# Kernel tuning notes

Hardware: AMD Instinct MI355X
Metric: run time of the kernel (lower is better)

The kernel has to match this reference:

```python
import jax, jax.numpy as jnp
import numpy as np

D_MODEL = 128
NEG_INF = -1e30


def setup_inputs() -> dict:
    key = jax.random.key(0)
    k1, k2, k3, k4 = jax.random.split(key, 4)
    B, Lc, Lq, d = 32, 2048, 256, D_MODEL
    C = jax.random.normal(k1, (B, Lc, d), dtype=jnp.float32)
    Q = jax.random.normal(k2, (B, Lq, d), dtype=jnp.float32)
    # Linear(3d, 1): weight laid out for cat order (Q_, C_, C_*Q_)
    w = jax.random.normal(k3, (3 * d,), dtype=jnp.float32) / np.sqrt(3 * d)
    b = jax.random.normal(k4, (1,), dtype=jnp.float32) * 0.01
    c_mask = jnp.ones((B, Lc), dtype=jnp.int32)
    q_mask = jnp.ones((B, Lq), dtype=jnp.int32)
    return {"C": C, "Q": Q, "w": w, "b": b, "c_mask": c_mask, "q_mask": q_mask}


def reference(C, Q, w, b, c_mask, q_mask):
    d = C.shape[-1]
    # Algebraic decomposition of Linear([Q_, C_, C_*Q_]) -> scalar:
    # S[b,i,j] = Q[b,j]@w_q + C[b,i]@w_c + (C[b,i]*w_m)@Q[b,j] + bias
    w_q, w_c, w_m = w[:d], w[d:2 * d], w[2 * d:]
    S = (C @ w_c)[:, :, None] \
        + (Q @ w_q)[:, None, :] \
        + jnp.einsum('bid,bjd->bij', C * w_m, Q) \
        + b[0]                                        # (B, Lc, Lq)
    mask = (c_mask[:, :, None] * q_mask[:, None, :]).astype(S.dtype)
    S = S * mask + NEG_INF * (1.0 - mask)
    S1 = jax.nn.softmax(S, axis=1)  # softmax over context dim (as in source)
    S2 = jax.nn.softmax(S, axis=2)  # softmax over query dim
    C2Q = jnp.einsum('bij,bjd->bid', S1, Q)           # (B, Lc, d)
    # Q2C = S1 @ S2^T @ C, associated as S1 @ (S2^T @ C) to avoid (Lc,Lc)
    T = jnp.einsum('bkj,bkd->bjd', S2, C)             # (B, Lq, d)
    Q2C = jnp.einsum('bij,bjd->bid', S1, T)           # (B, Lc, d)
    out = jnp.concatenate([C, C2Q, C * C2Q, C * Q2C], axis=2)  # (B, Lc, 4d)
    # dropout omitted (deterministic reference / eval mode)
    return out
```

## Files before the change

### kernel.cpp

```cpp
#include <hip/hip_runtime.h>


#define LC 2048
#define LQ 256
#define DM 128
#define NEG_INF_F (-1e30f)

using bf16x8  = __attribute__((ext_vector_type(8))) __bf16;
using f32x4   = __attribute__((ext_vector_type(4))) float;
using ushort8 = __attribute__((ext_vector_type(8))) unsigned short;

__device__ __forceinline__ unsigned short f2bf(float x) {
    unsigned int u = __float_as_uint(x);
    u += 0x7fffu + ((u >> 16) & 1u);
    return (unsigned short)(u >> 16);
}
__device__ __forceinline__ float bf2f(unsigned short h) {
    return __uint_as_float(((unsigned int)h) << 16);
}
__device__ __forceinline__ f32x4 mfma16(bf16x8 a, bf16x8 b, f32x4 c) {
    return __builtin_amdgcn_mfma_f32_16x16x32_bf16(a, b, c, 0, 0, 0);
}

__global__ __launch_bounds__(256) void k_preQ(const float* __restrict__ Q,
        const float* __restrict__ w, unsigned short* __restrict__ Qbf,
        unsigned short* __restrict__ Qt, float* __restrict__ rq) {
    const int b = blockIdx.z, j0 = blockIdx.x * 64, d0 = blockIdx.y * 64;
    const int tid = threadIdx.x;
    __shared__ float tile[64][65];
    __shared__ float wq[128];
    if (tid < 128) wq[tid] = w[tid];
    __syncthreads();
    const int r = tid >> 2, c0 = (tid & 3) * 16;
    const float4* sp = (const float4*)(Q + (size_t)(b * LQ + j0 + r) * DM + d0 + c0);
    float v[16];
#pragma unroll
    for (int u = 0; u < 4; ++u) {
        float4 t = sp[u];
        v[4*u] = t.x; v[4*u+1] = t.y; v[4*u+2] = t.z; v[4*u+3] = t.w;
    }
    unsigned short ob[16];
    float p = 0.f;
#pragma unroll
    for (int u = 0; u < 16; ++u) {
        ob[u] = f2bf(v[u]);
        p += v[u] * wq[d0 + c0 + u];
        tile[r][c0 + u] = v[u];
    }
    ushort8* qb = (ushort8*)(Qbf + (size_t)(b * LQ + j0 + r) * DM + d0 + c0);
    qb[0] = *(ushort8*)&ob[0];
    qb[1] = *(ushort8*)&ob[8];
    p += __shfl_xor(p, 1);
    p += __shfl_xor(p, 2);
    if ((tid & 3) == 0) atomicAdd(&rq[b * LQ + j0 + r], p);
    __syncthreads();
    unsigned short o[16];
#pragma unroll
    for (int u = 0; u < 16; ++u) o[u] = f2bf(tile[c0 + u][r]);
    ushort8* dp = (ushort8*)(Qt + (size_t)(b * DM + d0 + r) * LQ + j0 + c0);
    dp[0] = *(ushort8*)&o[0];
    dp[1] = *(ushort8*)&o[8];
}

__global__ __launch_bounds__(256) void k_preC(const float* __restrict__ C,
        unsigned short* __restrict__ Ct) {
    const int b = blockIdx.z, i0 = blockIdx.x * 64, d0 = blockIdx.y * 64;
    const int tid = threadIdx.x;
    __shared__ float tile[64][65];
    const int r = tid >> 2, c0 = (tid & 3) * 16;
    const float4* sp = (const float4*)(C + (size_t)(b * LC + i0 + r) * DM + d0 + c0);
#pragma unroll
    for (int u = 0; u < 4; ++u) {
        float4 t = sp[u];
        tile[r][c0 + 4*u] = t.x; tile[r][c0 + 4*u + 1] = t.y;
        tile[r][c0 + 4*u + 2] = t.z; tile[r][c0 + 4*u + 3] = t.w;
    }
    __syncthreads();
    unsigned short o[16];
#pragma unroll
    for (int u = 0; u < 16; ++u) o[u] = f2bf(tile[c0 + u][r]);
    ushort8* dp = (ushort8*)(Ct + (size_t)(b * DM + d0 + r) * LC + i0 + c0);
    dp[0] = *(ushort8*)&o[0];
    dp[1] = *(ushort8*)&o[8];
}

__global__ __launch_bounds__(256) void k1_scores(
    const float* __restrict__ C, const unsigned short* __restrict__ Qbf,
    const float* __restrict__ w, const float* __restrict__ bptr,
    const int* __restrict__ c_mask, const int* __restrict__ q_mask,
    const float* __restrict__ rq,
    unsigned short* __restrict__ E, float* __restrict__ l1g, float* __restrict__ l2g) {
    const int b = blockIdx.y;
    const int i0 = blockIdx.x * 64;
    const int tid = threadIdx.x;
    const int lane = tid & 63, wid = tid >> 6;
    const int quad = lane >> 4, l15 = lane & 15;

    __shared__ unsigned short Alds[64][136];
    __shared__ float wsm[256];
    __shared__ float rcs[64], rqs[256], cms[64], qms[256], l2s[64];
    __shared__ float b0s;

    if (tid < 256) {
        wsm[tid] = w[128 + tid];
        rqs[tid] = rq[b * LQ + tid];
        qms[tid] = (float)q_mask[b * LQ + tid];
    }
    if (tid < 64) {
        cms[tid] = (float)c_mask[b * LC + i0 + tid];
        l2s[tid] = 0.f;
    }
    if (tid == 0) b0s = bptr[0];
    __syncthreads();

    {
        const int r = tid >> 2, qq = tid & 3;
        const float4* cp = (const float4*)(C + (size_t)(b * LC + i0 + r) * DM + qq * 32);
        float prc = 0.f;
#pragma unroll
        for (int u = 0; u < 8; ++u) {
            float4 v = cp[u];
            const int c0 = qq * 32 + u * 4;
            prc += v.x * wsm[c0] + v.y * wsm[c0 + 1] + v.z * wsm[c0 + 2] + v.w * wsm[c0 + 3];
            Alds[r][c0 + 0] = f2bf(v.x * wsm[128 + c0]);
            Alds[r][c0 + 1] = f2bf(v.y * wsm[129 + c0]);
            Alds[r][c0 + 2] = f2bf(v.z * wsm[130 + c0]);
            Alds[r][c0 + 3] = f2bf(v.w * wsm[131 + c0]);
        }
        prc += __shfl_xor(prc, 1);
        prc += __shfl_xor(prc, 2);
        if (qq == 0) rcs[r] = prc;
    }
    __syncthreads();

    const int n_base = wid * 64;
    const unsigned short* qbase = Qbf + (size_t)b * LQ * DM;
    const f32x4 z4 = {0.f, 0.f, 0.f, 0.f};
    f32x4 acc[4][4];
#pragma unroll
    for (int mt = 0; mt < 4; ++mt)
#pragma unroll
        for (int nt = 0; nt < 4; ++nt) acc[mt][nt] = z4;

#pragma unroll
    for (int kc = 0; kc < 4; ++kc) {
        const int ko = kc * 32 + quad * 8;
        bf16x8 af[4], bfr[4];
#pragma unroll
        for (int mt = 0; mt < 4; ++mt)
            af[mt] = *(const bf16x8*)&Alds[mt * 16 + l15][ko];
#pragma unroll
        for (int nt = 0; nt < 4; ++nt)
            bfr[nt] = *(const bf16x8*)(qbase + (size_t)(n_base + nt * 16 + l15) * DM + ko);
#pragma unroll
        for (int mt = 0; mt < 4; ++mt)
#pragma unroll
            for (int nt = 0; nt < 4; ++nt)
                acc[mt][nt] = mfma16(af[mt], bfr[nt], acc[mt][nt]);
    }

    const float b0 = b0s;
    float colsum[4] = {0.f, 0.f, 0.f, 0.f};
#pragma unroll
    for (int mt = 0; mt < 4; ++mt) {
#pragma unroll
        for (int reg = 0; reg < 4; ++reg) {
            const int m = mt * 16 + quad * 4 + reg;
            float rowsum = 0.f;
#pragma unroll
            for (int nt = 0; nt < 4; ++nt) {
                const int n = n_base + nt * 16 + l15;
                float s = acc[mt][nt][reg] + rcs[m] + rqs[n] + b0;
                const float mk = cms[m] * qms[n];
                s = s * mk + NEG_INF_F * (1.f - mk);
                const float e = __expf(s);
                acc[mt][nt][reg] = e;
                rowsum += e;
                colsum[nt] += e;
            }
            rowsum += __shfl_xor(rowsum, 1);
            rowsum += __shfl_xor(rowsum, 2);
            rowsum += __shfl_xor(rowsum, 4);
            rowsum += __shfl_xor(rowsum, 8);
            if (l15 == 0) atomicAdd(&l2s[m], rowsum);
        }
    }
#pragma unroll
    for (int nt = 0; nt < 4; ++nt) {
        float v = colsum[nt];
        v += __shfl_xor(v, 16);
        v += __shfl_xor(v, 32);
        if (quad == 0) atomicAdd(&l1g[b * LQ + n_base + nt * 16 + l15], v);
    }
    __syncthreads();
    if (tid < 64) l2g[b * LC + i0 + tid] = l2s[tid];

#pragma unroll
    for (int mt = 0; mt < 4; ++mt) {
#pragma unroll
        for (int reg = 0; reg < 4; ++reg) {
            const int m = mt * 16 + quad * 4 + reg;
            const float rl = 1.0f / l2s[m];
            unsigned short* erow = E + (size_t)(b * LC + i0 + m) * LQ;
#pragma unroll
            for (int nt = 0; nt < 4; ++nt) {
                const int n = n_base + nt * 16 + l15;
                erow[n] = f2bf(acc[mt][nt][reg] * rl);
            }
        }
    }
}

__global__ __launch_bounds__(256) void kS_scaleQt(
    const unsigned short* __restrict__ Qt, const float* __restrict__ l1g,
    unsigned short* __restrict__ Qts) {
    const int b = blockIdx.y;
    const int tid = threadIdx.x;
    __shared__ float rl1s[256];
    rl1s[tid] = 1.0f / l1g[b * LQ + tid];
    __syncthreads();
    const int idx = blockIdx.x * 256 + tid;
    const int d = idx >> 5, jc = (idx & 31) * 8;
    const ushort8 v = *(const ushort8*)(Qt + (size_t)(b * DM + d) * LQ + jc);
    unsigned short o[8];
#pragma unroll
    for (int u = 0; u < 8; ++u) o[u] = f2bf(bf2f(v[u]) * rl1s[jc + u]);
    *(ushort8*)(Qts + (size_t)(b * DM + d) * LQ + jc) = *(ushort8*)&o[0];
}

__global__ __launch_bounds__(512) void k3_Tt(
    const unsigned short* __restrict__ E, const unsigned short* __restrict__ Ct,
    const float* __restrict__ l1g, unsigned short* __restrict__ Tt) {
    const int j0 = blockIdx.x * 64, d0 = blockIdx.y * 64, b = blockIdx.z;
    const int tid = threadIdx.x;
    const int lane = tid & 63, wid = tid >> 6;
    const int quad = lane >> 4, l15 = lane & 15;
    const int m_base = (wid >> 1) * 16, n32 = (wid & 1) * 32;

    __shared__ unsigned short Ab[64][136];
    __shared__ unsigned short Bb[64][136];
    __shared__ float rl1s[64];
    if (tid < 64) rl1s[tid] = 1.0f / l1g[b * LQ + j0 + tid];

    const f32x4 z4 = {0.f, 0.f, 0.f, 0.f};
    f32x4 acc[2] = {z4, z4};

    for (int it = 0; it < 16; ++it) {
        const int ic = it * 128;
        __syncthreads();
        {
            const int r = tid >> 3, q = tid & 7;
            const ushort8* cp = (const ushort8*)(Ct + (size_t)(b * DM + d0 + r) * LC + ic + q * 16);
            *(ushort8*)&Ab[r][q * 16] = cp[0];
            *(ushort8*)&Ab[r][q * 16 + 8] = cp[1];
        }
        {
            const int il = tid >> 2, sg = (tid & 3) * 16;
            const ushort8* ep = (const ushort8*)(E + (size_t)(b * LC + ic + il) * LQ + j0 + sg);
            ushort8 e0 = ep[0], e1 = ep[1];
#pragma unroll
            for (int u = 0; u < 8; ++u) Bb[sg + u][il] = e0[u];
#pragma unroll
            for (int u = 0; u < 8; ++u) Bb[sg + 8 + u][il] = e1[u];
        }
        __syncthreads();
#pragma unroll
        for (int kk = 0; kk < 4; ++kk) {
            const int ko = kk * 32 + quad * 8;
            bf16x8 af = *(const bf16x8*)&Ab[m_base + l15][ko];
            bf16x8 b0f = *(const bf16x8*)&Bb[n32 + l15][ko];
            bf16x8 b1f = *(const bf16x8*)&Bb[n32 + 16 + l15][ko];
            acc[0] = mfma16(af, b0f, acc[0]);
            acc[1] = mfma16(af, b1f, acc[1]);
        }
    }
#pragma unroll
    for (int nt = 0; nt < 2; ++nt)
#pragma unroll
        for (int reg = 0; reg < 4; ++reg) {
            const int dd = d0 + m_base + quad * 4 + reg;
            const int jl = n32 + nt * 16 + l15;
            Tt[(size_t)(b * DM + dd) * LQ + j0 + jl] = f2bf(acc[nt][reg] * rl1s[jl]);
        }
}

__global__ __launch_bounds__(256) void k4_out(
    const unsigned short* __restrict__ E, const float* __restrict__ C,
    const unsigned short* __restrict__ Qts, const unsigned short* __restrict__ Tt,
    const float* __restrict__ l2g, float* __restrict__ out) {
    const int b = blockIdx.y;
    const int i0 = blockIdx.x * 64;
    const int tid = threadIdx.x;
    const int lane = tid & 63, wid = tid >> 6;
    const int quad = lane >> 4, l15 = lane & 15;
    const int n_base = wid * 32;

    __shared__ unsigned short Aq[64][72];
    __shared__ unsigned short Bq[128][72];
    __shared__ unsigned short Bt2[128][72];
    __shared__ float l2s[64];
    if (tid < 64) l2s[tid] = l2g[b * LC + i0 + tid];

    const f32x4 z4 = {0.f, 0.f, 0.f, 0.f};
    f32x4 acc1[4][2], acc2[4][2];
#pragma unroll
    for (int mt = 0; mt < 4; ++mt)
#pragma unroll
        for (int nt = 0; nt < 2; ++nt) { acc1[mt][nt] = z4; acc2[mt][nt] = z4; }

#pragma unroll 1
    for (int kc = 0; kc < 4; ++kc) {
        const int jc = kc * 64;
        __syncthreads();
        {
            const int r = tid >> 2, q = tid & 3;
            const ushort8* ep = (const ushort8*)(E + (size_t)(b * LC + i0 + r) * LQ + jc + q * 16);
            *(ushort8*)&Aq[r][q * 16] = ep[0];
            *(ushort8*)&Aq[r][q * 16 + 8] = ep[1];
        }
        {
            const int r = tid >> 1, h = (tid & 1) * 32;
            const ushort8* qp = (const ushort8*)(Qts + (size_t)(b * DM + r) * LQ + jc + h);
            const ushort8* tp = (const ushort8*)(Tt + (size_t)(b * DM + r) * LQ + jc + h);
#pragma unroll
            for (int u = 0; u < 4; ++u) {
                *(ushort8*)&Bq[r][h + u * 8] = qp[u];
                *(ushort8*)&Bt2[r][h + u * 8] = tp[u];
            }
        }
        __syncthreads();
#pragma unroll
        for (int kk = 0; kk < 2; ++kk) {
            const int ko = kk * 32 + quad * 8;
            bf16x8 a[4], bq[2], bt[2];
#pragma unroll
            for (int mt = 0; mt < 4; ++mt)
                a[mt] = *(const bf16x8*)&Aq[mt * 16 + l15][ko];
#pragma unroll
            for (int nt = 0; nt < 2; ++nt) {
                bq[nt] = *(const bf16x8*)&Bq[n_base + nt * 16 + l15][ko];
                bt[nt] = *(const bf16x8*)&Bt2[n_base + nt * 16 + l15][ko];
            }
#pragma unroll
            for (int mt = 0; mt < 4; ++mt)
#pragma unroll
                for (int nt = 0; nt < 2; ++nt) {
                    acc1[mt][nt] = mfma16(a[mt], bq[nt], acc1[mt][nt]);
                    acc2[mt][nt] = mfma16(a[mt], bt[nt], acc2[mt][nt]);
                }
        }
    }

#pragma unroll
    for (int mt = 0; mt < 4; ++mt)
#pragma unroll
        for (int reg = 0; reg < 4; ++reg) {
            const int il = mt * 16 + quad * 4 + reg;
            const int i = i0 + il;
            const float l2v = l2s[il];
            const size_t rb = (size_t)(b * LC + i) * 512;
            const float* crow = C + (size_t)(b * LC + i) * DM;
#pragma unroll
            for (int nt = 0; nt < 2; ++nt) {
                const int d = n_base + nt * 16 + l15;
                const float c = crow[d];
                const float v1 = acc1[mt][nt][reg] * l2v;
                const float v2 = acc2[mt][nt][reg] * l2v;
                out[rb + d] = c;
                out[rb + 128 + d] = v1;
                out[rb + 256 + d] = c * v1;
                out[rb + 384 + d] = c * v2;
            }
        }
}

extern "C" void kernel_launch(void* const* d_in, const int* in_sizes, int n_in,
                              void* d_out, int out_size, void* d_ws, size_t ws_size,
                              hipStream_t stream) {
    const float* C = (const float*)d_in[0];
    const float* Q = (const float*)d_in[1];
    const float* w = (const float*)d_in[2];
    const float* bp = (const float*)d_in[3];
    const int* cm = (const int*)d_in[4];
    const int* qm = (const int*)d_in[5];
    float* out = (float*)d_out;

    char* ws = (char*)d_ws;
    unsigned short* E   = (unsigned short*)(ws);
    unsigned short* Ct  = (unsigned short*)(ws + 33554432);
    unsigned short* Qbf = (unsigned short*)(ws + 50331648);
    unsigned short* Qt  = (unsigned short*)(ws + 52428800);
    unsigned short* Qts = (unsigned short*)(ws + 54525952);
    unsigned short* Tt  = (unsigned short*)(ws + 56623104);
    float*          l2g = (float*)(ws + 58720256);
    float*          rq  = (float*)(ws + 58982400);
    float*          l1  = (float*)(ws + 59015168);

    hipMemsetAsync(ws + 58982400, 0, 65536, stream);

    k_preQ<<<dim3(4, 2, 32), 256, 0, stream>>>(Q, w, Qbf, Qt, rq);
    k_preC<<<dim3(32, 2, 32), 256, 0, stream>>>(C, Ct);
    k1_scores<<<dim3(32, 32), 256, 0, stream>>>(C, Qbf, w, bp, cm, qm, rq, E, l1, l2g);
    kS_scaleQt<<<dim3(16, 32), 256, 0, stream>>>(Qt, l1, Qts);
    k3_Tt<<<dim3(4, 2, 32), 512, 0, stream>>>(E, Ct, l1, Tt);
    k4_out<<<dim3(32, 32), 256, 0, stream>>>(E, C, Qts, Tt, l2g, out);
}
```

Before: 255.3 us.

## Emit transposed E from score kernel to vectorize Tt GEMM loads

The score kernel now stages each half of its normalized E tile in shared memory. It writes E row-major with vector stores and also writes a transposed copy Et. The Tt kernel then loads Et tiles with contiguous 16-byte loads, replacing the scalar scattered transposing stores into LDS. In exchange, k1 does an extra 32 MB bf16 write and adds syncs, and the workspace grows to hold Et.

```diff
diff --git a/kernel.cpp b/kernel.cpp
--- a/kernel.cpp
+++ b/kernel.cpp
@@ -89,7 +89,8 @@
     const float* __restrict__ w, const float* __restrict__ bptr,
     const int* __restrict__ c_mask, const int* __restrict__ q_mask,
     const float* __restrict__ rq,
-    unsigned short* __restrict__ E, float* __restrict__ l1g, float* __restrict__ l2g) {
+    unsigned short* __restrict__ E, unsigned short* __restrict__ Et,
+    float* __restrict__ l1g, float* __restrict__ l2g) {
     const int b = blockIdx.y;
     const int i0 = blockIdx.x * 64;
     const int tid = threadIdx.x;
@@ -196,17 +197,40 @@
     if (tid < 64) l2g[b * LC + i0 + tid] = l2s[tid];
 
 #pragma unroll
-    for (int mt = 0; mt < 4; ++mt) {
-#pragma unroll
-        for (int reg = 0; reg < 4; ++reg) {
-            const int m = mt * 16 + quad * 4 + reg;
-            const float rl = 1.0f / l2s[m];
-            unsigned short* erow = E + (size_t)(b * LC + i0 + m) * LQ;
-#pragma unroll
-            for (int nt = 0; nt < 4; ++nt) {
-                const int n = n_base + nt * 16 + l15;
-                erow[n] = f2bf(acc[mt][nt][reg] * rl);
+    for (int h = 0; h < 2; ++h) {
+        __syncthreads();
+        if ((wid >> 1) == h) {
+            const int ncol0 = (wid & 1) * 64;
+#pragma unroll
+            for (int mt = 0; mt < 4; ++mt)
+#pragma unroll
+            for (int reg = 0; reg < 4; ++reg) {
+                const int m = mt * 16 + quad * 4 + reg;
+                const float rl = 1.0f / l2s[m];
+#pragma unroll
+                for (int nt = 0; nt < 4; ++nt)
+                    Alds[m][ncol0 + nt * 16 + l15] = f2bf(acc[mt][nt][reg] * rl);
             }
+        }
+        __syncthreads();
+        {
+            const int r = tid >> 2, c0 = (tid & 3) * 32;
+            unsigned short* erow = E + (size_t)(b * LC + i0 + r) * LQ + h * 128 + c0;
+            *(ushort8*)(erow)      = *(const ushort8*)&Alds[r][c0];
+            *(ushort8*)(erow + 8)  = *(const ushort8*)&Alds[r][c0 + 8];
+            *(ushort8*)(erow + 16) = *(const ushort8*)&Alds[r][c0 + 16];
+            *(ushort8*)(erow + 24) = *(const ushort8*)&Alds[r][c0 + 24];
+        }
+        {
+            const int jl = tid >> 1, ih = (tid & 1) * 32;
+            unsigned short o[32];
+#pragma unroll
+            for (int u = 0; u < 32; ++u) o[u] = Alds[ih + u][jl];
+            unsigned short* trow = Et + (size_t)(b * LQ + h * 128 + jl) * LC + i0 + ih;
+            *(ushort8*)(trow)      = *(ushort8*)&o[0];
+            *(ushort8*)(trow + 8)  = *(ushort8*)&o[8];
+            *(ushort8*)(trow + 16) = *(ushort8*)&o[16];
+            *(ushort8*)(trow + 24) = *(ushort8*)&o[24];
         }
     }
 }
@@ -229,7 +253,7 @@
 }
 
 __global__ __launch_bounds__(512) void k3_Tt(
-    const unsigned short* __restrict__ E, const unsigned short* __restrict__ Ct,
+    const unsigned short* __restrict__ Et, const unsigned short* __restrict__ Ct,
     const float* __restrict__ l1g, unsigned short* __restrict__ Tt) {
     const int j0 = blockIdx.x * 64, d0 = blockIdx.y * 64, b = blockIdx.z;
     const int tid = threadIdx.x;
@@ -244,24 +268,18 @@
 
     const f32x4 z4 = {0.f, 0.f, 0.f, 0.f};
     f32x4 acc[2] = {z4, z4};
+    const int sr = tid >> 3, sq = tid & 7;
 
     for (int it = 0; it < 16; ++it) {
         const int ic = it * 128;
         __syncthreads();
         {
-            const int r = tid >> 3, q = tid & 7;
-            const ushort8* cp = (const ushort8*)(Ct + (size_t)(b * DM + d0 + r) * LC + ic + q * 16);
-            *(ushort8*)&Ab[r][q * 16] = cp[0];
-            *(ushort8*)&Ab[r][q * 16 + 8] = cp[1];
-        }
-        {
-            const int il = tid >> 2, sg = (tid & 3) * 16;
-            const ushort8* ep = (const ushort8*)(E + (size_t)(b * LC + ic + il) * LQ + j0 + sg);
-            ushort8 e0 = ep[0], e1 = ep[1];
-#pragma unroll
-            for (int u = 0; u < 8; ++u) Bb[sg + u][il] = e0[u];
-#pragma unroll
-            for (int u = 0; u < 8; ++u) Bb[sg + 8 + u][il] = e1[u];
+            const ushort8* cp = (const ushort8*)(Ct + (size_t)(b * DM + d0 + sr) * LC + ic + sq * 16);
+            *(ushort8*)&Ab[sr][sq * 16]     = cp[0];
+            *(ushort8*)&Ab[sr][sq * 16 + 8] = cp[1];
+            const ushort8* ep = (const ushort8*)(Et + (size_t)(b * LQ + j0 + sr) * LC + ic + sq * 16);
+            *(ushort8*)&Bb[sr][sq * 16]     = ep[0];
+            *(ushort8*)&Bb[sr][sq * 16 + 8] = ep[1];
         }
         __syncthreads();
 #pragma unroll
@@ -395,13 +413,14 @@
     float*          l2g = (float*)(ws + 58720256);
     float*          rq  = (float*)(ws + 58982400);
     float*          l1  = (float*)(ws + 59015168);
+    unsigned short* Et  = (unsigned short*)(ws + 59047936);
 
     hipMemsetAsync(ws + 58982400, 0, 65536, stream);
 
     k_preQ<<<dim3(4, 2, 32), 256, 0, stream>>>(Q, w, Qbf, Qt, rq);
     k_preC<<<dim3(32, 2, 32), 256, 0, stream>>>(C, Ct);
-    k1_scores<<<dim3(32, 32), 256, 0, stream>>>(C, Qbf, w, bp, cm, qm, rq, E, l1, l2g);
+    k1_scores<<<dim3(32, 32), 256, 0, stream>>>(C, Qbf, w, bp, cm, qm, rq, E, Et, l1, l2g);
     kS_scaleQt<<<dim3(16, 32), 256, 0, stream>>>(Qt, l1, Qts);
-    k3_Tt<<<dim3(4, 2, 32), 512, 0, stream>>>(E, Ct, l1, Tt);
+    k3_Tt<<<dim3(4, 2, 32), 512, 0, stream>>>(Et, Ct, l1, Tt);
     k4_out<<<dim3(32, 32), 256, 0, stream>>>(E, C, Qts, Tt, l2g, out);
 }
```

Result: slower. 273.4 us (+7.1%).

## Fuse C transpose into scores kernel and Q scaling into Tt kernel

Applied to the files above, without the earlier changes.

Drops the separate k_preC kernel: k1_scores now writes the bf16 transposed C (Ct) from the C values it already loads. Drops kS_scaleQt: k3_Tt blocks with dt==0 scale Qt by 1/l1 into Qts. k3_Tt also moves to a 1D grid that places consecutive block ids on different batches. The aim is to remove two launches and one extra read of C. The cost is that the Ct writes are now scalar 2-byte stores strided by LC, which coalesce poorly, and k3 gains an extra barrier and prologue work.

```diff
diff --git a/kernel.cpp b/kernel.cpp
--- a/kernel.cpp
+++ b/kernel.cpp
@@ -62,34 +62,13 @@
     dp[1] = *(ushort8*)&o[8];
 }
 
-__global__ __launch_bounds__(256) void k_preC(const float* __restrict__ C,
-        unsigned short* __restrict__ Ct) {
-    const int b = blockIdx.z, i0 = blockIdx.x * 64, d0 = blockIdx.y * 64;
-    const int tid = threadIdx.x;
-    __shared__ float tile[64][65];
-    const int r = tid >> 2, c0 = (tid & 3) * 16;
-    const float4* sp = (const float4*)(C + (size_t)(b * LC + i0 + r) * DM + d0 + c0);
-#pragma unroll
-    for (int u = 0; u < 4; ++u) {
-        float4 t = sp[u];
-        tile[r][c0 + 4*u] = t.x; tile[r][c0 + 4*u + 1] = t.y;
-        tile[r][c0 + 4*u + 2] = t.z; tile[r][c0 + 4*u + 3] = t.w;
-    }
-    __syncthreads();
-    unsigned short o[16];
-#pragma unroll
-    for (int u = 0; u < 16; ++u) o[u] = f2bf(tile[c0 + u][r]);
-    ushort8* dp = (ushort8*)(Ct + (size_t)(b * DM + d0 + r) * LC + i0 + c0);
-    dp[0] = *(ushort8*)&o[0];
-    dp[1] = *(ushort8*)&o[8];
-}
-
 __global__ __launch_bounds__(256) void k1_scores(
     const float* __restrict__ C, const unsigned short* __restrict__ Qbf,
     const float* __restrict__ w, const float* __restrict__ bptr,
     const int* __restrict__ c_mask, const int* __restrict__ q_mask,
     const float* __restrict__ rq,
-    unsigned short* __restrict__ E, float* __restrict__ l1g, float* __restrict__ l2g) {
+    unsigned short* __restrict__ E, unsigned short* __restrict__ Ct,
+    float* __restrict__ l1g, float* __restrict__ l2g) {
     const int b = blockIdx.y;
     const int i0 = blockIdx.x * 64;
     const int tid = threadIdx.x;
@@ -116,6 +95,7 @@
     {
         const int r = tid >> 2, qq = tid & 3;
         const float4* cp = (const float4*)(C + (size_t)(b * LC + i0 + r) * DM + qq * 32);
+        unsigned short* ctb = Ct + (size_t)b * DM * LC + i0 + r;
         float prc = 0.f;
 #pragma unroll
         for (int u = 0; u < 8; ++u) {
@@ -126,6 +106,10 @@
             Alds[r][c0 + 1] = f2bf(v.y * wsm[129 + c0]);
             Alds[r][c0 + 2] = f2bf(v.z * wsm[130 + c0]);
             Alds[r][c0 + 3] = f2bf(v.w * wsm[131 + c0]);
+            ctb[(size_t)(c0 + 0) * LC] = f2bf(v.x);
+            ctb[(size_t)(c0 + 1) * LC] = f2bf(v.y);
+            ctb[(size_t)(c0 + 2) * LC] = f2bf(v.z);
+            ctb[(size_t)(c0 + 3) * LC] = f2bf(v.w);
         }
         prc += __shfl_xor(prc, 1);
         prc += __shfl_xor(prc, 2);
@@ -211,27 +195,15 @@
     }
 }
 
-__global__ __launch_bounds__(256) void kS_scaleQt(
-    const unsigned short* __restrict__ Qt, const float* __restrict__ l1g,
-    unsigned short* __restrict__ Qts) {
-    const int b = blockIdx.y;
-    const int tid = threadIdx.x;
-    __shared__ float rl1s[256];
-    rl1s[tid] = 1.0f / l1g[b * LQ + tid];
-    __syncthreads();
-    const int idx = blockIdx.x * 256 + tid;
-    const int d = idx >> 5, jc = (idx & 31) * 8;
-    const ushort8 v = *(const ushort8*)(Qt + (size_t)(b * DM + d) * LQ + jc);
-    unsigned short o[8];
-#pragma unroll
-    for (int u = 0; u < 8; ++u) o[u] = f2bf(bf2f(v[u]) * rl1s[jc + u]);
-    *(ushort8*)(Qts + (size_t)(b * DM + d) * LQ + jc) = *(ushort8*)&o[0];
-}
-
 __global__ __launch_bounds__(512) void k3_Tt(
     const unsigned short* __restrict__ E, const unsigned short* __restrict__ Ct,
-    const float* __restrict__ l1g, unsigned short* __restrict__ Tt) {
-    const int j0 = blockIdx.x * 64, d0 = blockIdx.y * 64, b = blockIdx.z;
+    const unsigned short* __restrict__ Qt, const float* __restrict__ l1g,
+    unsigned short* __restrict__ Qts, unsigned short* __restrict__ Tt) {
+    const int id = blockIdx.x;
+    const int t = id >> 3;
+    const int jt = t & 3, dt = (t >> 2) & 1;
+    const int b = ((t >> 3) << 3) | (id & 7);
+    const int j0 = jt * 64, d0 = dt * 64;
     const int tid = threadIdx.x;
     const int lane = tid & 63, wid = tid >> 6;
     const int quad = lane >> 4, l15 = lane & 15;
@@ -241,6 +213,21 @@
     __shared__ unsigned short Bb[64][136];
     __shared__ float rl1s[64];
     if (tid < 64) rl1s[tid] = 1.0f / l1g[b * LQ + j0 + tid];
+    __syncthreads();
+
+    if (dt == 0) {
+        const int r = tid >> 2, jq = (tid & 3) * 16;
+        const ushort8* qp = (const ushort8*)(Qt + (size_t)(b * DM + r) * LQ + j0 + jq);
+        ushort8 v0 = qp[0], v1 = qp[1];
+        unsigned short o[16];
+#pragma unroll
+        for (int u = 0; u < 8; ++u) o[u] = f2bf(bf2f(v0[u]) * rl1s[jq + u]);
+#pragma unroll
+        for (int u = 0; u < 8; ++u) o[8 + u] = f2bf(bf2f(v1[u]) * rl1s[jq + 8 + u]);
+        ushort8* op = (ushort8*)(Qts + (size_t)(b * DM + r) * LQ + j0 + jq);
+        op[0] = *(ushort8*)&o[0];
+        op[1] = *(ushort8*)&o[8];
+    }
 
     const f32x4 z4 = {0.f, 0.f, 0.f, 0.f};
     f32x4 acc[2] = {z4, z4};
@@ -399,9 +386,7 @@
     hipMemsetAsync(ws + 58982400, 0, 65536, stream);
 
     k_preQ<<<dim3(4, 2, 32), 256, 0, stream>>>(Q, w, Qbf, Qt, rq);
-    k_preC<<<dim3(32, 2, 32), 256, 0, stream>>>(C, Ct);
-    k1_scores<<<dim3(32, 32), 256, 0, stream>>>(C, Qbf, w, bp, cm, qm, rq, E, l1, l2g);
-    kS_scaleQt<<<dim3(16, 32), 256, 0, stream>>>(Qt, l1, Qts);
-    k3_Tt<<<dim3(4, 2, 32), 512, 0, stream>>>(E, Ct, l1, Tt);
+    k1_scores<<<dim3(32, 32), 256, 0, stream>>>(C, Qbf, w, bp, cm, qm, rq, E, Ct, l1, l2g);
+    k3_Tt<<<dim3(256), 512, 0, stream>>>(E, Ct, Qt, l1, Qts, Tt);
     k4_out<<<dim3(32, 32), 256, 0, stream>>>(E, C, Qts, Tt, l2g, out);
 }
```

Measured after the change: 241.0 us. 5.6% less time.
